# Performance work log

Hardware: AMD Instinct MI355X
Metric: run time of the kernel (lower is better)

## Reference

```python
import jax, jax.numpy as jnp
import numpy as np

N, H, G = 8192, 256, 256


def setup_inputs() -> dict:
    key = jax.random.key(0)
    ks = jax.random.split(key, 12)
    s = 1.0 / np.sqrt(H)
    inp = {
        "x": jax.random.normal(ks[0], (N, H), dtype=jnp.float32),
        "batch": jnp.sort(jax.random.randint(ks[1], (N,), 0, G)),
        "num_graphs": G,
        "aw": jax.random.uniform(ks[2], (H, H), jnp.float32, -s, s),
        "ab": jax.random.uniform(ks[3], (H,), jnp.float32, -s, s),
        "p1w": jax.random.uniform(ks[4], (H, H), jnp.float32, -s, s),
        "p1b": jax.random.uniform(ks[5], (H,), jnp.float32, -s, s),
        "p2w": jax.random.uniform(ks[6], (H, H), jnp.float32, -s, s),
        "p2b": jax.random.uniform(ks[7], (H,), jnp.float32, -s, s),
        "r1w": jax.random.uniform(ks[8], (H, H), jnp.float32, -s, s),
        "r1b": jax.random.uniform(ks[9], (H,), jnp.float32, -s, s),
        "r2w": jax.random.uniform(ks[10], (H, H), jnp.float32, -s, s),
        "r2b": jax.random.uniform(ks[11], (H,), jnp.float32, -s, s),
    }
    return inp


def reference(x, batch, num_graphs, aw, ab, p1w, p1b, p2w, p2b, r1w, r1b, r2w, r2b):
    # phi: two Linear+ReLU layers
    h = jax.nn.relu(jax.nn.relu(x @ p1w + p1b) @ p2w + p2b)          # [N, H]
    s = h @ aw + ab                                                  # attention scores [N, H]
    dot = s @ s.T                                                    # [N, N]
    mask = (batch[:, None] == batch[None, :]).astype(dot.dtype)      # block-diagonal [N, N]
    # hand-rolled masked softmax exactly as in the torch module
    max_vals = jnp.max(dot * mask, axis=1, keepdims=True)            # [N, 1]
    masked_dot = (dot - max_vals) * mask
    e = jnp.exp(masked_dot)
    attn = e / jnp.sum(e * mask, axis=1, keepdims=True) * mask       # [N, N]
    x_weighted = attn @ h                                            # [N, H]
    x_agg = jax.ops.segment_sum(x_weighted, batch, num_segments=num_graphs)  # [G, H]
    # rho: two Linear+ReLU layers
    out = jax.nn.relu(jax.nn.relu(x_agg @ r1w + r1b) @ r2w + r2b)    # [G, H]
    return out
```

## Files before the change

kernel.cpp:

```cpp
#include <hip/hip_runtime.h>
#include <hip/hip_bf16.h>
#include <stdint.h>

#define NN 8192
#define HH 256
#define GG 256
#define PR 32

typedef __bf16 bf16x8 __attribute__((ext_vector_type(8)));
typedef float f32x4 __attribute__((ext_vector_type(4)));
typedef unsigned short u16v8 __attribute__((ext_vector_type(8)));

__device__ __forceinline__ ushort f2bf(float f) {
  union { float f; uint32_t u; } v; v.f = f;
  uint32_t u = v.u;
  u += 0x7fffu + ((u >> 16) & 1u);
  return (ushort)(u >> 16);
}
__device__ __forceinline__ float bf2f(ushort h) {
  union { uint32_t u; float f; } v; v.u = ((uint32_t)h) << 16;
  return v.f;
}

__global__ __launch_bounds__(256) void k_prep(const float* __restrict__ w0,
                                              const float* __restrict__ w1,
                                              const float* __restrict__ w2,
                                              const float* __restrict__ w3,
                                              const float* __restrict__ w4,
                                              ushort* __restrict__ o0,
                                              ushort* __restrict__ o1,
                                              ushort* __restrict__ o2,
                                              ushort* __restrict__ o3,
                                              ushort* __restrict__ o4,
                                              const int* __restrict__ batch,
                                              int* __restrict__ rs) {
  int b = blockIdx.x, t = threadIdx.x;
  if (b < 80) {
    int mat = b >> 4, tile = b & 15;
    int tr = (tile >> 2) * 64, tc = (tile & 3) * 64;
    const float* w = mat == 0 ? w0 : mat == 1 ? w1 : mat == 2 ? w2 : mat == 3 ? w3 : w4;
    ushort* o = mat == 0 ? o0 : mat == 1 ? o1 : mat == 2 ? o2 : mat == 3 ? o3 : o4;
    __shared__ float tileb[64][65];
    int rr = t >> 2, cg = (t & 3) * 16;
    const float* src = w + (size_t)(tr + rr) * HH + tc + cg;
#pragma unroll
    for (int j = 0; j < 4; ++j) {
      float4 v = *(const float4*)(src + j * 4);
      tileb[rr][cg + j * 4 + 0] = v.x;
      tileb[rr][cg + j * 4 + 1] = v.y;
      tileb[rr][cg + j * 4 + 2] = v.z;
      tileb[rr][cg + j * 4 + 3] = v.w;
    }
    __syncthreads();
    int rn = t >> 2, kg = (t & 3) * 16;
    u16v8 a, c;
#pragma unroll
    for (int j = 0; j < 8; ++j) a[j] = f2bf(tileb[kg + j][rn]);
#pragma unroll
    for (int j = 0; j < 8; ++j) c[j] = f2bf(tileb[kg + 8 + j][rn]);
    ushort* dst = o + (size_t)(tc + rn) * HH + tr + kg;
    *(u16v8*)dst = a;
    *(u16v8*)(dst + 8) = c;
  } else {
    for (int g = t; g <= GG; g += 256) {
      if (g == GG) { rs[GG] = NN; continue; }
      int lo = 0, hi = NN;
      while (lo < hi) { int mid = (lo + hi) >> 1; if (batch[mid] < g) lo = mid + 1; else hi = mid; }
      rs[g] = lo;
    }
  }
}

__device__ __forceinline__ void load_w_lds(const ushort* __restrict__ wt,
                                           ushort* wl, int tid) {
#pragma unroll
  for (int it = 0; it < 16; ++it) {
    int chunk = it * 512 + tid;
    int row = chunk >> 5, c = chunk & 31;
    int src = (chunk & ~31) | (c ^ (row & 7));
    __builtin_amdgcn_global_load_lds(
        (const __attribute__((address_space(1))) uint32_t*)(wt + src * 8),
        (__attribute__((address_space(3))) uint32_t*)(wl + chunk * 8),
        16, 0, 0);
  }
}

#define PHI_MFMA(ACC)                                                          \
  {                                                                            \
    _Pragma("unroll")                                                          \
    for (int kk = 0; kk < 8; ++kk) {                                           \
      int kc = (kk * 4 + q) ^ x7;                                              \
      bf16x8 a = *(const bf16x8*)(act + ((wr + l15) * 32 + kc) * 8);           \
      _Pragma("unroll")                                                        \
      for (int nt = 0; nt < 4; ++nt) {                                         \
        bf16x8 b = *(const bf16x8*)(wl + ((wc + nt * 16 + l15) * 32 + kc) * 8);\
        ACC[nt] = __builtin_amdgcn_mfma_f32_16x16x32_bf16(a, b, ACC[nt], 0, 0, 0); \
      }                                                                        \
    }                                                                          \
  }

__global__ __launch_bounds__(512, 1) void k_phi(const float* __restrict__ x,
    const ushort* __restrict__ wt1, const float* __restrict__ b1,
    const ushort* __restrict__ wt2, const float* __restrict__ b2,
    const ushort* __restrict__ wta, const float* __restrict__ ba,
    ushort* __restrict__ hb, ushort* __restrict__ sb) {
  __shared__ ushort wl[HH * HH];
  __shared__ ushort act[PR * HH];
  const int tid = threadIdx.x;
  const int rowbase = blockIdx.x * PR;

  load_w_lds(wt1, wl, tid);

#pragma unroll
  for (int it = 0; it < 2; ++it) {
    int chunk = it * 512 + tid;
    int row = chunk >> 5, c = chunk & 31;
    const float* xp = x + (size_t)(rowbase + row) * HH + c * 8;
    float4 v0 = *(const float4*)xp;
    float4 v1 = *(const float4*)(xp + 4);
    u16v8 o;
    o[0] = f2bf(v0.x); o[1] = f2bf(v0.y); o[2] = f2bf(v0.z); o[3] = f2bf(v0.w);
    o[4] = f2bf(v1.x); o[5] = f2bf(v1.y); o[6] = f2bf(v1.z); o[7] = f2bf(v1.w);
    int dst = (chunk & ~31) | (c ^ (row & 7));
    *(u16v8*)(act + dst * 8) = o;
  }
  __syncthreads();

  const int lane = tid & 63, wid = tid >> 6;
  const int l15 = lane & 15, q = lane >> 4, x7 = l15 & 7;
  const int wr = (wid & 1) * 16;
  const int wc = (wid >> 1) * 64;
  const int ro = wr + q * 4;

  f32x4 acc[4] = {{0.f,0.f,0.f,0.f},{0.f,0.f,0.f,0.f},{0.f,0.f,0.f,0.f},{0.f,0.f,0.f,0.f}};
  PHI_MFMA(acc);
  __syncthreads();
  load_w_lds(wt2, wl, tid);
#pragma unroll
  for (int nt = 0; nt < 4; ++nt) {
    int col = wc + nt * 16 + l15;
    float bv = b1[col];
#pragma unroll
    for (int i = 0; i < 4; ++i) {
      float v = fmaxf(acc[nt][i] + bv, 0.f);
      int r = ro + i;
      int cc = (col >> 3) ^ (r & 7);
      act[(r * 32 + cc) * 8 + (col & 7)] = f2bf(v);
    }
  }
  __syncthreads();

  f32x4 acc2[4] = {{0.f,0.f,0.f,0.f},{0.f,0.f,0.f,0.f},{0.f,0.f,0.f,0.f},{0.f,0.f,0.f,0.f}};
  PHI_MFMA(acc2);
  __syncthreads();
  load_w_lds(wta, wl, tid);
#pragma unroll
  for (int nt = 0; nt < 4; ++nt) {
    int col = wc + nt * 16 + l15;
    float bv = b2[col];
#pragma unroll
    for (int i = 0; i < 4; ++i) {
      float v = fmaxf(acc2[nt][i] + bv, 0.f);
      int r = ro + i;
      int cc = (col >> 3) ^ (r & 7);
      act[(r * 32 + cc) * 8 + (col & 7)] = f2bf(v);
    }
  }
  __syncthreads();

  f32x4 acc3[4] = {{0.f,0.f,0.f,0.f},{0.f,0.f,0.f,0.f},{0.f,0.f,0.f,0.f},{0.f,0.f,0.f,0.f}};
  PHI_MFMA(acc3);
#pragma unroll
  for (int nt = 0; nt < 4; ++nt) {
    int col = wc + nt * 16 + l15;
    float bv = ba[col];
#pragma unroll
    for (int i = 0; i < 4; ++i)
      sb[(size_t)(rowbase + ro + i) * HH + col] = f2bf(acc3[nt][i] + bv);
  }
#pragma unroll
  for (int it = 0; it < 2; ++it) {
    int chunk = it * 512 + tid;
    int row = chunk >> 5, c = chunk & 31;
    int srcp = (chunk & ~31) | (c ^ (row & 7));
    u16v8 v = *(const u16v8*)(act + srcp * 8);
    *(u16v8*)(hb + (size_t)rowbase * HH + chunk * 8) = v;
  }
}

__device__ __forceinline__ float dotbf(const ushort* __restrict__ a,
                                       const ushort* __restrict__ b) {
  float acc = 0.f;
  for (int k = 0; k < HH; k += 2) {
    acc = fmaf(bf2f(a[k]), bf2f(b[k]), acc);
    acc = fmaf(bf2f(a[k + 1]), bf2f(b[k + 1]), acc);
  }
  return acc;
}

__global__ __launch_bounds__(256) void k_attn(const ushort* __restrict__ sb,
                                              const ushort* __restrict__ h,
                                              const int* __restrict__ rs,
                                              float* __restrict__ xagg) {
  int g = blockIdx.x;
  int r0 = rs[g], r1 = rs[g + 1];
  int n = r1 - r0;
  __shared__ ushort st[64 * 256];
  __shared__ float colw[256];
  int tid = threadIdx.x;
  colw[tid] = 0.f;
  if (n <= 64) {
    for (int ch = tid; ch < n * 32; ch += 256) {
      int row = ch >> 5, c = ch & 31;
      int sc = (c ^ (row & 7)) << 4;
      ulonglong2 v = *(const ulonglong2*)(sb + (size_t)(r0 + row) * HH + c * 8);
      *(ulonglong2*)((char*)st + row * 512 + sc) = v;
    }
    __syncthreads();
    const int lane = tid & 63, wid = tid >> 6;
    const int l15 = lane & 15, q = lane >> 4;
    const int x7 = l15 & 7;
    const char* stc = (const char*)st;
    if (wid * 16 < n) {
      f32x4 acc0 = {0.f, 0.f, 0.f, 0.f};
      f32x4 acc1 = acc0, acc2 = acc0, acc3 = acc0;
      const int arow = wid * 16 + l15;
#pragma unroll
      for (int kk = 0; kk < 8; kk++) {
        int kc = ((kk * 4 + q) ^ x7) << 4;
        bf16x8 a  = *(const bf16x8*)(stc + arow * 512 + kc);
        bf16x8 b0 = *(const bf16x8*)(stc + l15 * 512 + kc);
        acc0 = __builtin_amdgcn_mfma_f32_16x16x32_bf16(a, b0, acc0, 0, 0, 0);
        if (n > 16) {
          bf16x8 b1 = *(const bf16x8*)(stc + (16 + l15) * 512 + kc);
          acc1 = __builtin_amdgcn_mfma_f32_16x16x32_bf16(a, b1, acc1, 0, 0, 0);
        }
        if (n > 32) {
          bf16x8 b2 = *(const bf16x8*)(stc + (32 + l15) * 512 + kc);
          acc2 = __builtin_amdgcn_mfma_f32_16x16x32_bf16(a, b2, acc2, 0, 0, 0);
        }
        if (n > 48) {
          bf16x8 b3 = *(const bf16x8*)(stc + (48 + l15) * 512 + kc);
          acc3 = __builtin_amdgcn_mfma_f32_16x16x32_bf16(a, b3, acc3, 0, 0, 0);
        }
      }
      float mi[4], e0[4], e1[4], e2[4], e3[4], inv[4];
#pragma unroll
      for (int i = 0; i < 4; i++) {
        float mm = (l15 < n) ? acc0[i] : -1e30f;
        if (16 + l15 < n) mm = fmaxf(mm, acc1[i]);
        if (32 + l15 < n) mm = fmaxf(mm, acc2[i]);
        if (48 + l15 < n) mm = fmaxf(mm, acc3[i]);
        mi[i] = mm;
      }
#pragma unroll
      for (int off = 1; off < 16; off <<= 1)
#pragma unroll
        for (int i = 0; i < 4; i++) mi[i] = fmaxf(mi[i], __shfl_xor(mi[i], off));
#pragma unroll
      for (int i = 0; i < 4; i++) {
        e0[i] = (l15 < n)      ? __expf(acc0[i] - mi[i]) : 0.f;
        e1[i] = (16 + l15 < n) ? __expf(acc1[i] - mi[i]) : 0.f;
        e2[i] = (32 + l15 < n) ? __expf(acc2[i] - mi[i]) : 0.f;
        e3[i] = (48 + l15 < n) ? __expf(acc3[i] - mi[i]) : 0.f;
        inv[i] = e0[i] + e1[i] + e2[i] + e3[i];
      }
#pragma unroll
      for (int off = 1; off < 16; off <<= 1)
#pragma unroll
        for (int i = 0; i < 4; i++) inv[i] += __shfl_xor(inv[i], off);
#pragma unroll
      for (int i = 0; i < 4; i++) inv[i] = 1.f / inv[i];
      float cs[4];
#pragma unroll
      for (int t = 0; t < 4; t++) {
        const float* et = t == 0 ? e0 : t == 1 ? e1 : t == 2 ? e2 : e3;
        float c4 = 0.f;
#pragma unroll
        for (int i = 0; i < 4; i++) {
          int row = wid * 16 + q * 4 + i;
          c4 += (row < n) ? et[i] * inv[i] : 0.f;
        }
        cs[t] = c4;
      }
#pragma unroll
      for (int t = 0; t < 4; t++) {
        cs[t] += __shfl_xor(cs[t], 16);
        cs[t] += __shfl_xor(cs[t], 32);
      }
      if (lane < 16) {
#pragma unroll
        for (int t = 0; t < 4; t++)
          if (t * 16 < n) atomicAdd(&colw[t * 16 + l15], cs[t]);
      }
    }
    __syncthreads();
  } else {
    int nn = n > 256 ? 256 : n;
    __syncthreads();
    int wid = tid >> 6, lane = tid & 63;
    for (int i = wid; i < nn; i += 4) {
      const ushort* si = sb + (size_t)(r0 + i) * HH;
      float d[4];
      int j[4];
#pragma unroll
      for (int u = 0; u < 4; u++) {
        j[u] = lane + u * 64;
        d[u] = (j[u] < nn) ? dotbf(si, sb + (size_t)(r0 + j[u]) * HH) : -1e30f;
      }
      float m = fmaxf(fmaxf(d[0], d[1]), fmaxf(d[2], d[3]));
#pragma unroll
      for (int off = 32; off; off >>= 1) m = fmaxf(m, __shfl_xor(m, off));
      float e[4], ss = 0.f;
#pragma unroll
      for (int u = 0; u < 4; u++) { e[u] = (j[u] < nn) ? __expf(d[u] - m) : 0.f; ss += e[u]; }
#pragma unroll
      for (int off = 32; off; off >>= 1) ss += __shfl_xor(ss, off);
      float iv = 1.f / ss;
#pragma unroll
      for (int u = 0; u < 4; u++)
        if (j[u] < nn) atomicAdd(&colw[j[u]], e[u] * iv);
    }
    __syncthreads();
  }
  int c = tid;
  int nn = n > 256 ? 256 : n;
  float agg = 0.f;
#pragma unroll 8
  for (int jj = 0; jj < nn; jj++)
    agg = fmaf(colw[jj], bf2f(h[(size_t)(r0 + jj) * HH + c]), agg);
  xagg[(size_t)g * HH + c] = agg;
}

__global__ __launch_bounds__(512, 1) void k_rho2(const float* __restrict__ xagg,
    const ushort* __restrict__ rt1, const float* __restrict__ b1,
    const ushort* __restrict__ rt2, const float* __restrict__ b2,
    float* __restrict__ out) {
  __shared__ ushort wl[HH * HH];
  __shared__ ushort act[PR * HH];
  const int tid = threadIdx.x;
  const int rowbase = blockIdx.x * PR;

  load_w_lds(rt1, wl, tid);

#pragma unroll
  for (int it = 0; it < 2; ++it) {
    int chunk = it * 512 + tid;
    int row = chunk >> 5, c = chunk & 31;
    const float* xp = xagg + (size_t)(rowbase + row) * HH + c * 8;
    float4 v0 = *(const float4*)xp;
    float4 v1 = *(const float4*)(xp + 4);
    u16v8 o;
    o[0] = f2bf(v0.x); o[1] = f2bf(v0.y); o[2] = f2bf(v0.z); o[3] = f2bf(v0.w);
    o[4] = f2bf(v1.x); o[5] = f2bf(v1.y); o[6] = f2bf(v1.z); o[7] = f2bf(v1.w);
    int dst = (chunk & ~31) | (c ^ (row & 7));
    *(u16v8*)(act + dst * 8) = o;
  }
  __syncthreads();

  const int lane = tid & 63, wid = tid >> 6;
  const int l15 = lane & 15, q = lane >> 4, x7 = l15 & 7;
  const int wr = (wid & 1) * 16;
  const int wc = (wid >> 1) * 64;
  const int ro = wr + q * 4;

  f32x4 acc[4] = {{0.f,0.f,0.f,0.f},{0.f,0.f,0.f,0.f},{0.f,0.f,0.f,0.f},{0.f,0.f,0.f,0.f}};
  PHI_MFMA(acc);
  __syncthreads();
  load_w_lds(rt2, wl, tid);
#pragma unroll
  for (int nt = 0; nt < 4; ++nt) {
    int col = wc + nt * 16 + l15;
    float bv = b1[col];
#pragma unroll
    for (int i = 0; i < 4; ++i) {
      float v = fmaxf(acc[nt][i] + bv, 0.f);
      int r = ro + i;
      int cc = (col >> 3) ^ (r & 7);
      act[(r * 32 + cc) * 8 + (col & 7)] = f2bf(v);
    }
  }
  __syncthreads();

  f32x4 acc2[4] = {{0.f,0.f,0.f,0.f},{0.f,0.f,0.f,0.f},{0.f,0.f,0.f,0.f},{0.f,0.f,0.f,0.f}};
  PHI_MFMA(acc2);
#pragma unroll
  for (int nt = 0; nt < 4; ++nt) {
    int col = wc + nt * 16 + l15;
    float bv = b2[col];
#pragma unroll
    for (int i = 0; i < 4; ++i)
      out[(size_t)(rowbase + ro + i) * HH + col] = fmaxf(acc2[nt][i] + bv, 0.f);
  }
}

extern "C" void kernel_launch(void* const* d_in, const int* in_sizes, int n_in,
                              void* d_out, int out_size, void* d_ws, size_t ws_size,
                              hipStream_t stream) {
  const float* x   = (const float*)d_in[0];
  const int* batch = (const int*)d_in[1];
  const float* aw  = (const float*)d_in[3];
  const float* ab  = (const float*)d_in[4];
  const float* p1w = (const float*)d_in[5];
  const float* p1b = (const float*)d_in[6];
  const float* p2w = (const float*)d_in[7];
  const float* p2b = (const float*)d_in[8];
  const float* r1w = (const float*)d_in[9];
  const float* r1b = (const float*)d_in[10];
  const float* r2w = (const float*)d_in[11];
  const float* r2b = (const float*)d_in[12];
  float* out = (float*)d_out;

  char* ws = (char*)d_ws;
  ushort* hb   = (ushort*)(ws);
  ushort* sb16 = (ushort*)(ws + (size_t)4 * 1024 * 1024);
  ushort* wT1  = (ushort*)(ws + (size_t)8 * 1024 * 1024);
  ushort* wT2  = wT1 + 65536;
  ushort* wTa  = wT2 + 65536;
  ushort* rT1  = wTa + 65536;
  ushort* rT2  = rT1 + 65536;
  float*  xagg = (float*)(ws + (size_t)8 * 1024 * 1024 + 640 * 1024);
  int*    rsb  = (int*)(ws + (size_t)8 * 1024 * 1024 + 896 * 1024);

  k_prep<<<dim3(81), dim3(256), 0, stream>>>(p1w, p2w, aw, r1w, r2w,
                                             wT1, wT2, wTa, rT1, rT2, batch, rsb);
  k_phi<<<dim3(256), dim3(512), 0, stream>>>(x, wT1, p1b, wT2, p2b, wTa, ab, hb, sb16);
  k_attn<<<dim3(256), dim3(256), 0, stream>>>(sb16, hb, rsb, xagg);
  k_rho2<<<dim3(8), dim3(512), 0, stream>>>(xagg, rT1, r1b, rT2, r2b, out);
}
```

Before: 38.38 us.

## Fuse prep, phi, attention and rho into one persistent kernel with grid barriers

Merges the four kernels into a single 256-block launch and replaces kernel boundaries with atomic-counter grid barriers in workspace flags, reset by a memset. The aim is to remove per-launch overhead and the idle gaps between stages. The attention stage now runs with 512 threads, so more waves share the dot-product rows and the final aggregation is split into two halves. This relies on all 256 blocks being co-resident (one block per CU at 144KB of LDS), otherwise the spin-waits deadlock, and it adds a memset plus spin-wait latency.

```diff
diff --git a/kernel.cpp b/kernel.cpp
--- a/kernel.cpp
+++ b/kernel.cpp
@@ -20,55 +20,6 @@
 __device__ __forceinline__ float bf2f(ushort h) {
   union { uint32_t u; float f; } v; v.u = ((uint32_t)h) << 16;
   return v.f;
-}
-
-__global__ __launch_bounds__(256) void k_prep(const float* __restrict__ w0,
-                                              const float* __restrict__ w1,
-                                              const float* __restrict__ w2,
-                                              const float* __restrict__ w3,
-                                              const float* __restrict__ w4,
-                                              ushort* __restrict__ o0,
-                                              ushort* __restrict__ o1,
-                                              ushort* __restrict__ o2,
-                                              ushort* __restrict__ o3,
-                                              ushort* __restrict__ o4,
-                                              const int* __restrict__ batch,
-                                              int* __restrict__ rs) {
-  int b = blockIdx.x, t = threadIdx.x;
-  if (b < 80) {
-    int mat = b >> 4, tile = b & 15;
-    int tr = (tile >> 2) * 64, tc = (tile & 3) * 64;
-    const float* w = mat == 0 ? w0 : mat == 1 ? w1 : mat == 2 ? w2 : mat == 3 ? w3 : w4;
-    ushort* o = mat == 0 ? o0 : mat == 1 ? o1 : mat == 2 ? o2 : mat == 3 ? o3 : o4;
-    __shared__ float tileb[64][65];
-    int rr = t >> 2, cg = (t & 3) * 16;
-    const float* src = w + (size_t)(tr + rr) * HH + tc + cg;
-#pragma unroll
-    for (int j = 0; j < 4; ++j) {
-      float4 v = *(const float4*)(src + j * 4);
-      tileb[rr][cg + j * 4 + 0] = v.x;
-      tileb[rr][cg + j * 4 + 1] = v.y;
-      tileb[rr][cg + j * 4 + 2] = v.z;
-      tileb[rr][cg + j * 4 + 3] = v.w;
-    }
-    __syncthreads();
-    int rn = t >> 2, kg = (t & 3) * 16;
-    u16v8 a, c;
-#pragma unroll
-    for (int j = 0; j < 8; ++j) a[j] = f2bf(tileb[kg + j][rn]);
-#pragma unroll
-    for (int j = 0; j < 8; ++j) c[j] = f2bf(tileb[kg + 8 + j][rn]);
-    ushort* dst = o + (size_t)(tc + rn) * HH + tr + kg;
-    *(u16v8*)dst = a;
-    *(u16v8*)(dst + 8) = c;
-  } else {
-    for (int g = t; g <= GG; g += 256) {
-      if (g == GG) { rs[GG] = NN; continue; }
-      int lo = 0, hi = NN;
-      while (lo < hi) { int mid = (lo + hi) >> 1; if (batch[mid] < g) lo = mid + 1; else hi = mid; }
-      rs[g] = lo;
-    }
-  }
 }
 
 __device__ __forceinline__ void load_w_lds(const ushort* __restrict__ wt,
@@ -93,24 +44,72 @@
       bf16x8 a = *(const bf16x8*)(act + ((wr + l15) * 32 + kc) * 8);           \
       _Pragma("unroll")                                                        \
       for (int nt = 0; nt < 4; ++nt) {                                         \
-        bf16x8 b = *(const bf16x8*)(wl + ((wc + nt * 16 + l15) * 32 + kc) * 8);\
-        ACC[nt] = __builtin_amdgcn_mfma_f32_16x16x32_bf16(a, b, ACC[nt], 0, 0, 0); \
+        bf16x8 bfr = *(const bf16x8*)(wl + ((wc + nt * 16 + l15) * 32 + kc) * 8);\
+        ACC[nt] = __builtin_amdgcn_mfma_f32_16x16x32_bf16(a, bfr, ACC[nt], 0, 0, 0); \
       }                                                                        \
     }                                                                          \
   }
 
-__global__ __launch_bounds__(512, 1) void k_phi(const float* __restrict__ x,
-    const ushort* __restrict__ wt1, const float* __restrict__ b1,
-    const ushort* __restrict__ wt2, const float* __restrict__ b2,
-    const ushort* __restrict__ wta, const float* __restrict__ ba,
-    ushort* __restrict__ hb, ushort* __restrict__ sb) {
-  __shared__ ushort wl[HH * HH];
-  __shared__ ushort act[PR * HH];
-  const int tid = threadIdx.x;
-  const int rowbase = blockIdx.x * PR;
-
-  load_w_lds(wt1, wl, tid);
-
+__device__ __forceinline__ float dotbf(const ushort* __restrict__ a,
+                                       const ushort* __restrict__ b) {
+  float acc = 0.f;
+  for (int k = 0; k < HH; k += 2) {
+    acc = fmaf(bf2f(a[k]), bf2f(b[k]), acc);
+    acc = fmaf(bf2f(a[k + 1]), bf2f(b[k + 1]), acc);
+  }
+  return acc;
+}
+
+__global__ __launch_bounds__(512, 1) void k_fused(
+    const float* __restrict__ x, const int* __restrict__ batch,
+    const float* __restrict__ aw, const float* __restrict__ ab,
+    const float* __restrict__ p1w, const float* __restrict__ p1b,
+    const float* __restrict__ p2w, const float* __restrict__ p2b,
+    const float* __restrict__ r1w, const float* __restrict__ r1b,
+    const float* __restrict__ r2w, const float* __restrict__ r2b,
+    ushort* __restrict__ hb, ushort* __restrict__ sb,
+    ushort* __restrict__ wT1, ushort* __restrict__ wT2, ushort* __restrict__ wTa,
+    ushort* __restrict__ rT1, ushort* __restrict__ rT2,
+    float* __restrict__ xagg, int* __restrict__ rs, int* __restrict__ flags,
+    float* __restrict__ out) {
+  __shared__ char smem[147456];
+  const int b = blockIdx.x, tid = threadIdx.x;
+  ushort* wl = (ushort*)smem;
+  ushort* act = (ushort*)(smem + 131072);
+
+  if (b < 80) {
+    int mat = b >> 4, tile = b & 15;
+    int tr = (tile >> 2) * 64, tc = (tile & 3) * 64;
+    const float* w = mat == 0 ? p1w : mat == 1 ? p2w : mat == 2 ? aw : mat == 3 ? r1w : r2w;
+    ushort* o = mat == 0 ? wT1 : mat == 1 ? wT2 : mat == 2 ? wTa : mat == 3 ? rT1 : rT2;
+    float* tileb = (float*)smem;
+    int rr = tid >> 3, cg = (tid & 7) * 8;
+    const float* src = w + (size_t)(tr + rr) * HH + tc + cg;
+    float4 v0 = *(const float4*)src;
+    float4 v1 = *(const float4*)(src + 4);
+    float* drow = tileb + rr * 65 + cg;
+    drow[0] = v0.x; drow[1] = v0.y; drow[2] = v0.z; drow[3] = v0.w;
+    drow[4] = v1.x; drow[5] = v1.y; drow[6] = v1.z; drow[7] = v1.w;
+    __syncthreads();
+    int rn = tid >> 3, kg = (tid & 7) * 8;
+    u16v8 a;
+#pragma unroll
+    for (int j = 0; j < 8; ++j) a[j] = f2bf(tileb[(kg + j) * 65 + rn]);
+    *(u16v8*)(o + (size_t)(tc + rn) * HH + tr + kg) = a;
+    __syncthreads();
+  } else if (b == 80) {
+    if (tid <= 256) {
+      int g = tid;
+      if (g == GG) { rs[GG] = NN; }
+      else {
+        int lo = 0, hi = NN;
+        while (lo < hi) { int mid = (lo + hi) >> 1; if (batch[mid] < g) lo = mid + 1; else hi = mid; }
+        rs[g] = lo;
+      }
+    }
+  }
+
+  const int rowbase = b * PR;
 #pragma unroll
   for (int it = 0; it < 2; ++it) {
     int chunk = it * 512 + tid;
@@ -124,273 +123,282 @@
     int dst = (chunk & ~31) | (c ^ (row & 7));
     *(u16v8*)(act + dst * 8) = o;
   }
-  __syncthreads();
-
-  const int lane = tid & 63, wid = tid >> 6;
-  const int l15 = lane & 15, q = lane >> 4, x7 = l15 & 7;
-  const int wr = (wid & 1) * 16;
-  const int wc = (wid >> 1) * 64;
-  const int ro = wr + q * 4;
-
-  f32x4 acc[4] = {{0.f,0.f,0.f,0.f},{0.f,0.f,0.f,0.f},{0.f,0.f,0.f,0.f},{0.f,0.f,0.f,0.f}};
-  PHI_MFMA(acc);
-  __syncthreads();
-  load_w_lds(wt2, wl, tid);
-#pragma unroll
-  for (int nt = 0; nt < 4; ++nt) {
-    int col = wc + nt * 16 + l15;
-    float bv = b1[col];
-#pragma unroll
-    for (int i = 0; i < 4; ++i) {
-      float v = fmaxf(acc[nt][i] + bv, 0.f);
-      int r = ro + i;
-      int cc = (col >> 3) ^ (r & 7);
-      act[(r * 32 + cc) * 8 + (col & 7)] = f2bf(v);
-    }
-  }
-  __syncthreads();
-
-  f32x4 acc2[4] = {{0.f,0.f,0.f,0.f},{0.f,0.f,0.f,0.f},{0.f,0.f,0.f,0.f},{0.f,0.f,0.f,0.f}};
-  PHI_MFMA(acc2);
-  __syncthreads();
-  load_w_lds(wta, wl, tid);
-#pragma unroll
-  for (int nt = 0; nt < 4; ++nt) {
-    int col = wc + nt * 16 + l15;
-    float bv = b2[col];
-#pragma unroll
-    for (int i = 0; i < 4; ++i) {
-      float v = fmaxf(acc2[nt][i] + bv, 0.f);
-      int r = ro + i;
-      int cc = (col >> 3) ^ (r & 7);
-      act[(r * 32 + cc) * 8 + (col & 7)] = f2bf(v);
-    }
-  }
-  __syncthreads();
-
-  f32x4 acc3[4] = {{0.f,0.f,0.f,0.f},{0.f,0.f,0.f,0.f},{0.f,0.f,0.f,0.f},{0.f,0.f,0.f,0.f}};
-  PHI_MFMA(acc3);
-#pragma unroll
-  for (int nt = 0; nt < 4; ++nt) {
-    int col = wc + nt * 16 + l15;
-    float bv = ba[col];
-#pragma unroll
-    for (int i = 0; i < 4; ++i)
-      sb[(size_t)(rowbase + ro + i) * HH + col] = f2bf(acc3[nt][i] + bv);
-  }
-#pragma unroll
-  for (int it = 0; it < 2; ++it) {
-    int chunk = it * 512 + tid;
-    int row = chunk >> 5, c = chunk & 31;
-    int srcp = (chunk & ~31) | (c ^ (row & 7));
-    u16v8 v = *(const u16v8*)(act + srcp * 8);
-    *(u16v8*)(hb + (size_t)rowbase * HH + chunk * 8) = v;
-  }
-}
-
-__device__ __forceinline__ float dotbf(const ushort* __restrict__ a,
-                                       const ushort* __restrict__ b) {
-  float acc = 0.f;
-  for (int k = 0; k < HH; k += 2) {
-    acc = fmaf(bf2f(a[k]), bf2f(b[k]), acc);
-    acc = fmaf(bf2f(a[k + 1]), bf2f(b[k + 1]), acc);
-  }
-  return acc;
-}
-
-__global__ __launch_bounds__(256) void k_attn(const ushort* __restrict__ sb,
-                                              const ushort* __restrict__ h,
-                                              const int* __restrict__ rs,
-                                              float* __restrict__ xagg) {
-  int g = blockIdx.x;
-  int r0 = rs[g], r1 = rs[g + 1];
-  int n = r1 - r0;
-  __shared__ ushort st[64 * 256];
-  __shared__ float colw[256];
-  int tid = threadIdx.x;
-  colw[tid] = 0.f;
-  if (n <= 64) {
-    for (int ch = tid; ch < n * 32; ch += 256) {
-      int row = ch >> 5, c = ch & 31;
-      int sc = (c ^ (row & 7)) << 4;
-      ulonglong2 v = *(const ulonglong2*)(sb + (size_t)(r0 + row) * HH + c * 8);
-      *(ulonglong2*)((char*)st + row * 512 + sc) = v;
-    }
-    __syncthreads();
+
+  __syncthreads();
+  if (tid == 0) {
+    if (b < 80)
+      __hip_atomic_fetch_add(flags + 0, 1, __ATOMIC_RELEASE, __HIP_MEMORY_SCOPE_AGENT);
+    while (__hip_atomic_load(flags + 0, __ATOMIC_ACQUIRE, __HIP_MEMORY_SCOPE_AGENT) < 80)
+      __builtin_amdgcn_s_sleep(2);
+  }
+  __syncthreads();
+
+  {
+    load_w_lds(wT1, wl, tid);
+    __syncthreads();
+
     const int lane = tid & 63, wid = tid >> 6;
-    const int l15 = lane & 15, q = lane >> 4;
-    const int x7 = l15 & 7;
-    const char* stc = (const char*)st;
-    if (wid * 16 < n) {
-      f32x4 acc0 = {0.f, 0.f, 0.f, 0.f};
-      f32x4 acc1 = acc0, acc2 = acc0, acc3 = acc0;
-      const int arow = wid * 16 + l15;
-#pragma unroll
-      for (int kk = 0; kk < 8; kk++) {
-        int kc = ((kk * 4 + q) ^ x7) << 4;
-        bf16x8 a  = *(const bf16x8*)(stc + arow * 512 + kc);
-        bf16x8 b0 = *(const bf16x8*)(stc + l15 * 512 + kc);
-        acc0 = __builtin_amdgcn_mfma_f32_16x16x32_bf16(a, b0, acc0, 0, 0, 0);
-        if (n > 16) {
-          bf16x8 b1 = *(const bf16x8*)(stc + (16 + l15) * 512 + kc);
-          acc1 = __builtin_amdgcn_mfma_f32_16x16x32_bf16(a, b1, acc1, 0, 0, 0);
-        }
-        if (n > 32) {
-          bf16x8 b2 = *(const bf16x8*)(stc + (32 + l15) * 512 + kc);
-          acc2 = __builtin_amdgcn_mfma_f32_16x16x32_bf16(a, b2, acc2, 0, 0, 0);
-        }
-        if (n > 48) {
-          bf16x8 b3 = *(const bf16x8*)(stc + (48 + l15) * 512 + kc);
-          acc3 = __builtin_amdgcn_mfma_f32_16x16x32_bf16(a, b3, acc3, 0, 0, 0);
-        }
-      }
-      float mi[4], e0[4], e1[4], e2[4], e3[4], inv[4];
-#pragma unroll
-      for (int i = 0; i < 4; i++) {
-        float mm = (l15 < n) ? acc0[i] : -1e30f;
-        if (16 + l15 < n) mm = fmaxf(mm, acc1[i]);
-        if (32 + l15 < n) mm = fmaxf(mm, acc2[i]);
-        if (48 + l15 < n) mm = fmaxf(mm, acc3[i]);
-        mi[i] = mm;
-      }
-#pragma unroll
-      for (int off = 1; off < 16; off <<= 1)
-#pragma unroll
-        for (int i = 0; i < 4; i++) mi[i] = fmaxf(mi[i], __shfl_xor(mi[i], off));
-#pragma unroll
-      for (int i = 0; i < 4; i++) {
-        e0[i] = (l15 < n)      ? __expf(acc0[i] - mi[i]) : 0.f;
-        e1[i] = (16 + l15 < n) ? __expf(acc1[i] - mi[i]) : 0.f;
-        e2[i] = (32 + l15 < n) ? __expf(acc2[i] - mi[i]) : 0.f;
-        e3[i] = (48 + l15 < n) ? __expf(acc3[i] - mi[i]) : 0.f;
-        inv[i] = e0[i] + e1[i] + e2[i] + e3[i];
-      }
-#pragma unroll
-      for (int off = 1; off < 16; off <<= 1)
-#pragma unroll
-        for (int i = 0; i < 4; i++) inv[i] += __shfl_xor(inv[i], off);
-#pragma unroll
-      for (int i = 0; i < 4; i++) inv[i] = 1.f / inv[i];
-      float cs[4];
-#pragma unroll
-      for (int t = 0; t < 4; t++) {
-        const float* et = t == 0 ? e0 : t == 1 ? e1 : t == 2 ? e2 : e3;
-        float c4 = 0.f;
+    const int l15 = lane & 15, q = lane >> 4, x7 = l15 & 7;
+    const int wr = (wid & 1) * 16;
+    const int wc = (wid >> 1) * 64;
+    const int ro = wr + q * 4;
+
+    f32x4 acc[4] = {{0.f,0.f,0.f,0.f},{0.f,0.f,0.f,0.f},{0.f,0.f,0.f,0.f},{0.f,0.f,0.f,0.f}};
+    PHI_MFMA(acc);
+    __syncthreads();
+    load_w_lds(wT2, wl, tid);
+#pragma unroll
+    for (int nt = 0; nt < 4; ++nt) {
+      int col = wc + nt * 16 + l15;
+      float bv = p1b[col];
+#pragma unroll
+      for (int i = 0; i < 4; ++i) {
+        float v = fmaxf(acc[nt][i] + bv, 0.f);
+        int r = ro + i;
+        int cc = (col >> 3) ^ (r & 7);
+        act[(r * 32 + cc) * 8 + (col & 7)] = f2bf(v);
+      }
+    }
+    __syncthreads();
+
+    f32x4 acc2[4] = {{0.f,0.f,0.f,0.f},{0.f,0.f,0.f,0.f},{0.f,0.f,0.f,0.f},{0.f,0.f,0.f,0.f}};
+    PHI_MFMA(acc2);
+    __syncthreads();
+    load_w_lds(wTa, wl, tid);
+#pragma unroll
+    for (int nt = 0; nt < 4; ++nt) {
+      int col = wc + nt * 16 + l15;
+      float bv = p2b[col];
+#pragma unroll
+      for (int i = 0; i < 4; ++i) {
+        float v = fmaxf(acc2[nt][i] + bv, 0.f);
+        int r = ro + i;
+        int cc = (col >> 3) ^ (r & 7);
+        act[(r * 32 + cc) * 8 + (col & 7)] = f2bf(v);
+      }
+    }
+    __syncthreads();
+
+    f32x4 acc3[4] = {{0.f,0.f,0.f,0.f},{0.f,0.f,0.f,0.f},{0.f,0.f,0.f,0.f},{0.f,0.f,0.f,0.f}};
+    PHI_MFMA(acc3);
+#pragma unroll
+    for (int nt = 0; nt < 4; ++nt) {
+      int col = wc + nt * 16 + l15;
+      float bv = ab[col];
+#pragma unroll
+      for (int i = 0; i < 4; ++i)
+        sb[(size_t)(rowbase + ro + i) * HH + col] = f2bf(acc3[nt][i] + bv);
+    }
+#pragma unroll
+    for (int it = 0; it < 2; ++it) {
+      int chunk = it * 512 + tid;
+      int row = chunk >> 5, c = chunk & 31;
+      int srcp = (chunk & ~31) | (c ^ (row & 7));
+      u16v8 v = *(const u16v8*)(act + srcp * 8);
+      *(u16v8*)(hb + (size_t)rowbase * HH + chunk * 8) = v;
+    }
+  }
+
+  __syncthreads();
+  if (tid == 0) {
+    __hip_atomic_fetch_add(flags + 1, 1, __ATOMIC_RELEASE, __HIP_MEMORY_SCOPE_AGENT);
+    while (__hip_atomic_load(flags + 1, __ATOMIC_ACQUIRE, __HIP_MEMORY_SCOPE_AGENT) < 256)
+      __builtin_amdgcn_s_sleep(2);
+  }
+  __syncthreads();
+
+  {
+    int g = b;
+    int r0 = rs[g], r1 = rs[g + 1];
+    int n = r1 - r0;
+    ushort* st = (ushort*)smem;
+    float* colw = (float*)(smem + 32768);
+    float* agg2 = (float*)(smem + 32768 + 1024);
+    if (tid < 256) colw[tid] = 0.f;
+    const int lane = tid & 63, wid = tid >> 6;
+    const int l15 = lane & 15, q = lane >> 4, x7 = l15 & 7;
+    if (n <= 64) {
+      for (int ch = tid; ch < n * 32; ch += 512) {
+        int row = ch >> 5, c = ch & 31;
+        int sc = (c ^ (row & 7)) << 4;
+        ulonglong2 v = *(const ulonglong2*)(sb + (size_t)(r0 + row) * HH + c * 8);
+        *(ulonglong2*)((char*)st + row * 512 + sc) = v;
+      }
+      __syncthreads();
+      const char* stc = (const char*)st;
+      if (wid < 4 && wid * 16 < n) {
+        f32x4 acc0 = {0.f, 0.f, 0.f, 0.f};
+        f32x4 acc1 = acc0, acc2 = acc0, acc3 = acc0;
+        const int arow = wid * 16 + l15;
+#pragma unroll
+        for (int kk = 0; kk < 8; kk++) {
+          int kc = ((kk * 4 + q) ^ x7) << 4;
+          bf16x8 a  = *(const bf16x8*)(stc + arow * 512 + kc);
+          bf16x8 b0 = *(const bf16x8*)(stc + l15 * 512 + kc);
+          acc0 = __builtin_amdgcn_mfma_f32_16x16x32_bf16(a, b0, acc0, 0, 0, 0);
+          if (n > 16) {
+            bf16x8 b1 = *(const bf16x8*)(stc + (16 + l15) * 512 + kc);
+            acc1 = __builtin_amdgcn_mfma_f32_16x16x32_bf16(a, b1, acc1, 0, 0, 0);
+          }
+          if (n > 32) {
+            bf16x8 b2 = *(const bf16x8*)(stc + (32 + l15) * 512 + kc);
+            acc2 = __builtin_amdgcn_mfma_f32_16x16x32_bf16(a, b2, acc2, 0, 0, 0);
+          }
+          if (n > 48) {
+            bf16x8 b3 = *(const bf16x8*)(stc + (48 + l15) * 512 + kc);
+            acc3 = __builtin_amdgcn_mfma_f32_16x16x32_bf16(a, b3, acc3, 0, 0, 0);
+          }
+        }
+        float mi[4], e0[4], e1[4], e2[4], e3[4], inv[4];
 #pragma unroll
         for (int i = 0; i < 4; i++) {
-          int row = wid * 16 + q * 4 + i;
-          c4 += (row < n) ? et[i] * inv[i] : 0.f;
-        }
-        cs[t] = c4;
-      }
-#pragma unroll
-      for (int t = 0; t < 4; t++) {
-        cs[t] += __shfl_xor(cs[t], 16);
-        cs[t] += __shfl_xor(cs[t], 32);
-      }
-      if (lane < 16) {
-#pragma unroll
-        for (int t = 0; t < 4; t++)
-          if (t * 16 < n) atomicAdd(&colw[t * 16 + l15], cs[t]);
-      }
-    }
-    __syncthreads();
-  } else {
+          float mm = (l15 < n) ? acc0[i] : -1e30f;
+          if (16 + l15 < n) mm = fmaxf(mm, acc1[i]);
+          if (32 + l15 < n) mm = fmaxf(mm, acc2[i]);
+          if (48 + l15 < n) mm = fmaxf(mm, acc3[i]);
+          mi[i] = mm;
+        }
+#pragma unroll
+        for (int off = 1; off < 16; off <<= 1)
+#pragma unroll
+          for (int i = 0; i < 4; i++) mi[i] = fmaxf(mi[i], __shfl_xor(mi[i], off));
+#pragma unroll
+        for (int i = 0; i < 4; i++) {
+          e0[i] = (l15 < n)      ? __expf(acc0[i] - mi[i]) : 0.f;
+          e1[i] = (16 + l15 < n) ? __expf(acc1[i] - mi[i]) : 0.f;
+          e2[i] = (32 + l15 < n) ? __expf(acc2[i] - mi[i]) : 0.f;
+          e3[i] = (48 + l15 < n) ? __expf(acc3[i] - mi[i]) : 0.f;
+          inv[i] = e0[i] + e1[i] + e2[i] + e3[i];
+        }
+#pragma unroll
+        for (int off = 1; off < 16; off <<= 1)
+#pragma unroll
+          for (int i = 0; i < 4; i++) inv[i] += __shfl_xor(inv[i], off);
+#pragma unroll
+        for (int i = 0; i < 4; i++) inv[i] = 1.f / inv[i];
+        float cs[4];
+#pragma unroll
+        for (int t = 0; t < 4; t++) {
+          const float* et = t == 0 ? e0 : t == 1 ? e1 : t == 2 ? e2 : e3;
+          float c4 = 0.f;
+#pragma unroll
+          for (int i = 0; i < 4; i++) {
+            int row = wid * 16 + q * 4 + i;
+            c4 += (row < n) ? et[i] * inv[i] : 0.f;
+          }
+          cs[t] = c4;
+        }
+#pragma unroll
+        for (int t = 0; t < 4; t++) {
+          cs[t] += __shfl_xor(cs[t], 16);
+          cs[t] += __shfl_xor(cs[t], 32);
+        }
+        if (lane < 16) {
+#pragma unroll
+          for (int t = 0; t < 4; t++)
+            if (t * 16 < n) atomicAdd(&colw[t * 16 + l15], cs[t]);
+        }
+      }
+      __syncthreads();
+    } else {
+      int nn = n > 256 ? 256 : n;
+      __syncthreads();
+      for (int i = wid; i < nn; i += 8) {
+        const ushort* si = sb + (size_t)(r0 + i) * HH;
+        float d[4];
+        int j[4];
+#pragma unroll
+        for (int u = 0; u < 4; u++) {
+          j[u] = lane + u * 64;
+          d[u] = (j[u] < nn) ? dotbf(si, sb + (size_t)(r0 + j[u]) * HH) : -1e30f;
+        }
+        float m = fmaxf(fmaxf(d[0], d[1]), fmaxf(d[2], d[3]));
+#pragma unroll
+        for (int off = 32; off; off >>= 1) m = fmaxf(m, __shfl_xor(m, off));
+        float e[4], ss = 0.f;
+#pragma unroll
+        for (int u = 0; u < 4; u++) { e[u] = (j[u] < nn) ? __expf(d[u] - m) : 0.f; ss += e[u]; }
+#pragma unroll
+        for (int off = 32; off; off >>= 1) ss += __shfl_xor(ss, off);
+        float iv = 1.f / ss;
+#pragma unroll
+        for (int u = 0; u < 4; u++)
+          if (j[u] < nn) atomicAdd(&colw[j[u]], e[u] * iv);
+      }
+      __syncthreads();
+    }
+    int c = tid & 255, half = tid >> 8;
     int nn = n > 256 ? 256 : n;
-    __syncthreads();
-    int wid = tid >> 6, lane = tid & 63;
-    for (int i = wid; i < nn; i += 4) {
-      const ushort* si = sb + (size_t)(r0 + i) * HH;
-      float d[4];
-      int j[4];
-#pragma unroll
-      for (int u = 0; u < 4; u++) {
-        j[u] = lane + u * 64;
-        d[u] = (j[u] < nn) ? dotbf(si, sb + (size_t)(r0 + j[u]) * HH) : -1e30f;
-      }
-      float m = fmaxf(fmaxf(d[0], d[1]), fmaxf(d[2], d[3]));
-#pragma unroll
-      for (int off = 32; off; off >>= 1) m = fmaxf(m, __shfl_xor(m, off));
-      float e[4], ss = 0.f;
-#pragma unroll
-      for (int u = 0; u < 4; u++) { e[u] = (j[u] < nn) ? __expf(d[u] - m) : 0.f; ss += e[u]; }
-#pragma unroll
-      for (int off = 32; off; off >>= 1) ss += __shfl_xor(ss, off);
-      float iv = 1.f / ss;
-#pragma unroll
-      for (int u = 0; u < 4; u++)
-        if (j[u] < nn) atomicAdd(&colw[j[u]], e[u] * iv);
-    }
-    __syncthreads();
-  }
-  int c = tid;
-  int nn = n > 256 ? 256 : n;
-  float agg = 0.f;
-#pragma unroll 8
-  for (int jj = 0; jj < nn; jj++)
-    agg = fmaf(colw[jj], bf2f(h[(size_t)(r0 + jj) * HH + c]), agg);
-  xagg[(size_t)g * HH + c] = agg;
-}
-
-__global__ __launch_bounds__(512, 1) void k_rho2(const float* __restrict__ xagg,
-    const ushort* __restrict__ rt1, const float* __restrict__ b1,
-    const ushort* __restrict__ rt2, const float* __restrict__ b2,
-    float* __restrict__ out) {
-  __shared__ ushort wl[HH * HH];
-  __shared__ ushort act[PR * HH];
-  const int tid = threadIdx.x;
-  const int rowbase = blockIdx.x * PR;
-
-  load_w_lds(rt1, wl, tid);
-
-#pragma unroll
-  for (int it = 0; it < 2; ++it) {
-    int chunk = it * 512 + tid;
-    int row = chunk >> 5, c = chunk & 31;
-    const float* xp = xagg + (size_t)(rowbase + row) * HH + c * 8;
-    float4 v0 = *(const float4*)xp;
-    float4 v1 = *(const float4*)(xp + 4);
-    u16v8 o;
-    o[0] = f2bf(v0.x); o[1] = f2bf(v0.y); o[2] = f2bf(v0.z); o[3] = f2bf(v0.w);
-    o[4] = f2bf(v1.x); o[5] = f2bf(v1.y); o[6] = f2bf(v1.z); o[7] = f2bf(v1.w);
-    int dst = (chunk & ~31) | (c ^ (row & 7));
-    *(u16v8*)(act + dst * 8) = o;
-  }
-  __syncthreads();
-
-  const int lane = tid & 63, wid = tid >> 6;
-  const int l15 = lane & 15, q = lane >> 4, x7 = l15 & 7;
-  const int wr = (wid & 1) * 16;
-  const int wc = (wid >> 1) * 64;
-  const int ro = wr + q * 4;
-
-  f32x4 acc[4] = {{0.f,0.f,0.f,0.f},{0.f,0.f,0.f,0.f},{0.f,0.f,0.f,0.f},{0.f,0.f,0.f,0.f}};
-  PHI_MFMA(acc);
-  __syncthreads();
-  load_w_lds(rt2, wl, tid);
-#pragma unroll
-  for (int nt = 0; nt < 4; ++nt) {
-    int col = wc + nt * 16 + l15;
-    float bv = b1[col];
-#pragma unroll
-    for (int i = 0; i < 4; ++i) {
-      float v = fmaxf(acc[nt][i] + bv, 0.f);
-      int r = ro + i;
-      int cc = (col >> 3) ^ (r & 7);
-      act[(r * 32 + cc) * 8 + (col & 7)] = f2bf(v);
-    }
-  }
-  __syncthreads();
-
-  f32x4 acc2[4] = {{0.f,0.f,0.f,0.f},{0.f,0.f,0.f,0.f},{0.f,0.f,0.f,0.f},{0.f,0.f,0.f,0.f}};
-  PHI_MFMA(acc2);
-#pragma unroll
-  for (int nt = 0; nt < 4; ++nt) {
-    int col = wc + nt * 16 + l15;
-    float bv = b2[col];
-#pragma unroll
-    for (int i = 0; i < 4; ++i)
-      out[(size_t)(rowbase + ro + i) * HH + col] = fmaxf(acc2[nt][i] + bv, 0.f);
+    float agg = 0.f;
+    for (int jj = half; jj < nn; jj += 2)
+      agg = fmaf(colw[jj], bf2f(hb[(size_t)(r0 + jj) * HH + c]), agg);
+    agg2[half * 256 + c] = agg;
+    __syncthreads();
+    if (tid < 256) xagg[(size_t)g * HH + tid] = agg2[tid] + agg2[256 + tid];
+  }
+
+  __syncthreads();
+  if (tid == 0)
+    __hip_atomic_fetch_add(flags + 2, 1, __ATOMIC_RELEASE, __HIP_MEMORY_SCOPE_AGENT);
+  if (b >= 8) return;
+  if (tid == 0) {
+    while (__hip_atomic_load(flags + 2, __ATOMIC_ACQUIRE, __HIP_MEMORY_SCOPE_AGENT) < 256)
+      __builtin_amdgcn_s_sleep(2);
+  }
+  __syncthreads();
+
+  {
+    const int rowb = b * PR;
+    load_w_lds(rT1, wl, tid);
+#pragma unroll
+    for (int it = 0; it < 2; ++it) {
+      int chunk = it * 512 + tid;
+      int row = chunk >> 5, c = chunk & 31;
+      const float* xp = xagg + (size_t)(rowb + row) * HH + c * 8;
+      float4 v0 = *(const float4*)xp;
+      float4 v1 = *(const float4*)(xp + 4);
+      u16v8 o;
+      o[0] = f2bf(v0.x); o[1] = f2bf(v0.y); o[2] = f2bf(v0.z); o[3] = f2bf(v0.w);
+      o[4] = f2bf(v1.x); o[5] = f2bf(v1.y); o[6] = f2bf(v1.z); o[7] = f2bf(v1.w);
+      int dst = (chunk & ~31) | (c ^ (row & 7));
+      *(u16v8*)(act + dst * 8) = o;
+    }
+    __syncthreads();
+
+    const int lane = tid & 63, wid = tid >> 6;
+    const int l15 = lane & 15, q = lane >> 4, x7 = l15 & 7;
+    const int wr = (wid & 1) * 16;
+    const int wc = (wid >> 1) * 64;
+    const int ro = wr + q * 4;
+
+    f32x4 acc[4] = {{0.f,0.f,0.f,0.f},{0.f,0.f,0.f,0.f},{0.f,0.f,0.f,0.f},{0.f,0.f,0.f,0.f}};
+    PHI_MFMA(acc);
+    __syncthreads();
+    load_w_lds(rT2, wl, tid);
+#pragma unroll
+    for (int nt = 0; nt < 4; ++nt) {
+      int col = wc + nt * 16 + l15;
+      float bv = r1b[col];
+#pragma unroll
+      for (int i = 0; i < 4; ++i) {
+        float v = fmaxf(acc[nt][i] + bv, 0.f);
+        int r = ro + i;
+        int cc = (col >> 3) ^ (r & 7);
+        act[(r * 32 + cc) * 8 + (col & 7)] = f2bf(v);
+      }
+    }
+    __syncthreads();
+
+    f32x4 acc2[4] = {{0.f,0.f,0.f,0.f},{0.f,0.f,0.f,0.f},{0.f,0.f,0.f,0.f},{0.f,0.f,0.f,0.f}};
+    PHI_MFMA(acc2);
+#pragma unroll
+    for (int nt = 0; nt < 4; ++nt) {
+      int col = wc + nt * 16 + l15;
+      float bv = r2b[col];
+#pragma unroll
+      for (int i = 0; i < 4; ++i)
+        out[(size_t)(rowb + ro + i) * HH + col] = fmaxf(acc2[nt][i] + bv, 0.f);
+    }
   }
 }
 
@@ -421,10 +429,10 @@
   ushort* rT2  = rT1 + 65536;
   float*  xagg = (float*)(ws + (size_t)8 * 1024 * 1024 + 640 * 1024);
   int*    rsb  = (int*)(ws + (size_t)8 * 1024 * 1024 + 896 * 1024);
-
-  k_prep<<<dim3(81), dim3(256), 0, stream>>>(p1w, p2w, aw, r1w, r2w,
-                                             wT1, wT2, wTa, rT1, rT2, batch, rsb);
-  k_phi<<<dim3(256), dim3(512), 0, stream>>>(x, wT1, p1b, wT2, p2b, wTa, ab, hb, sb16);
-  k_attn<<<dim3(256), dim3(256), 0, stream>>>(sb16, hb, rsb, xagg);
-  k_rho2<<<dim3(8), dim3(512), 0, stream>>>(xagg, rT1, r1b, rT2, r2b, out);
-}
+  int*    flags = (int*)(ws + (size_t)8 * 1024 * 1024 + 900 * 1024);
+
+  (void)hipMemsetAsync(flags, 0, 16, stream);
+  k_fused<<<dim3(256), dim3(512), 0, stream>>>(
+      x, batch, aw, ab, p1w, p1b, p2w, p2b, r1w, r1b, r2w, r2b,
+      hb, sb16, wT1, wT2, wTa, rT1, rT2, xagg, rsb, flags, out);
+}
```

Measured after the change: 75.08 us. 95.6% more time.
